# Kernel optimization log

Hardware: AMD Instinct MI355X
Metric: run time of the kernel (lower is better)

## Reference

```python
import jax, jax.numpy as jnp
import numpy as np

EPS = 1e-8


def setup_inputs() -> dict:
    key = jax.random.key(0)
    k1, k2, k3, k4 = jax.random.split(key, 4)
    b, c_in, c_out, h, w_, k = 16, 512, 512, 64, 64, 3
    return {
        "x": jax.random.normal(k1, (b, c_in, h, w_), dtype=jnp.float32),
        "w": jax.random.normal(k2, (b, 512), dtype=jnp.float32),
        "weight": jax.random.normal(k3, (c_out, c_in, k, k), dtype=jnp.float32),
        "affine_w": jax.random.normal(k4, (c_in, 512), dtype=jnp.float32) * 0.02,
        "affine_b": jnp.zeros((c_in,), dtype=jnp.float32),
    }


def reference(x, w, weight, affine_w, affine_b):
    # x: [b, c_in, h, w]; w: [b, 512]; weight: [c_out, c_in, k, k]
    b = x.shape[0]
    # per-sample modulation scale: [b, c_in]
    s = w @ affine_w.T + affine_b + 1.0
    # modulated weights: [b, c_out, c_in, k, k]
    wgt = weight[None] * s[:, None, :, None, None]
    # demodulation: rsqrt of sum over (c_in, kh, kw)
    d = jax.lax.rsqrt(jnp.sum(wgt ** 2, axis=(2, 3, 4)) + EPS)  # [b, c_out]
    wgt = wgt * d[:, :, None, None, None]

    def conv_one(x_i, w_i):
        # x_i: [c_in, h, w] -> [1, c_in, h, w]; w_i: [c_out, c_in, k, k]
        out = jax.lax.conv_general_dilated(
            x_i[None], w_i, window_strides=(1, 1), padding="SAME",
            dimension_numbers=("NCHW", "OIHW", "NCHW"))
        return out[0]

    return jax.vmap(conv_one)(x, wgt)  # [b, c_out, h, w]
```

## Files before the change

kernel.cpp:

```cpp
#include <hip/hip_runtime.h>
#include <cstdint>

typedef __bf16 bf16_t;
typedef __attribute__((ext_vector_type(8))) __bf16 bf16x8;
typedef __attribute__((ext_vector_type(4))) float f32x4;

#define MC_EPS 1e-8f

__device__ __forceinline__ void async_ld16(const bf16_t* g, bf16_t* l) {
  __builtin_amdgcn_global_load_lds(
      (const __attribute__((address_space(1))) void*)g,
      (__attribute__((address_space(3))) void*)l, 16, 0, 0);
}

__global__ void s_kernel(const float* __restrict__ w, const float* __restrict__ aw,
                         const float* __restrict__ ab, float* __restrict__ s) {
  int ci = blockIdx.x, tid = threadIdx.x;
  int b = tid >> 4, part = tid & 15;
  const float* ar = aw + (ci << 9);
  const float* wr = w + (b << 9);
  float acc = 0.f;
  for (int j = part; j < 512; j += 16) acc += wr[j] * ar[j];
  for (int off = 8; off; off >>= 1) acc += __shfl_down(acc, off, 64);
  if (part == 0) s[(b << 9) + ci] = acc + ab[ci] + 1.0f;
}

__global__ void prep_w_kernel(const float* __restrict__ wgt, float* __restrict__ wsq,
                              bf16_t* __restrict__ w_t) {
  int idx = blockIdx.x * 256 + threadIdx.x;
  const float* p = wgt + (size_t)idx * 9;
  float v[9];
  float a = 0.f;
#pragma unroll
  for (int j = 0; j < 9; ++j) { v[j] = p[j]; a += v[j] * v[j]; }
  wsq[idx] = a;
#pragma unroll
  for (int j = 0; j < 9; ++j) w_t[((size_t)j << 18) + idx] = (bf16_t)v[j];
}

__global__ void d_kernel(const float* __restrict__ wsq, const float* __restrict__ s,
                         float* __restrict__ d) {
  int co = blockIdx.x, tid = threadIdx.x;
  int b = tid >> 4, part = tid & 15;
  const float* wr = wsq + (co << 9);
  const float* sr = s + (b << 9);
  float acc = 0.f;
  for (int j = part; j < 512; j += 16) { float sv = sr[j]; acc += wr[j] * sv * sv; }
  for (int off = 8; off; off >>= 1) acc += __shfl_down(acc, off, 64);
  if (part == 0) d[(b << 9) + co] = rsqrtf(acc + MC_EPS);
}

__global__ void halo_kernel(bf16_t* __restrict__ xp) {
  int gid = blockIdx.x * 256 + threadIdx.x;
  if (gid >= 16 * 260 * 64) return;
  int cg = gid & 63;
  int p = (gid >> 6) % 260;
  int b = (gid >> 6) / 260;
  int h, w;
  if (p < 66)       { h = 0;       w = p; }
  else if (p < 132) { h = 65;      w = p - 66; }
  else if (p < 196) { h = p - 131; w = 0; }
  else              { h = p - 195; w = 65; }
  uint4 z = {0u, 0u, 0u, 0u};
  *(uint4*)&xp[((size_t)(b * 66 + h) * 66 + w) * 512 + (cg << 3)] = z;
}

__global__ void xmod_kernel(const float* __restrict__ x, const float* __restrict__ s,
                            bf16_t* __restrict__ xp) {
  int b = blockIdx.x >> 6, h = blockIdx.x & 63;
  int tid = threadIdx.x;
  __shared__ __align__(16) bf16_t tile[64 * 130];
  for (int c0 = 0; c0 < 512; c0 += 128) {
    if (c0) __syncthreads();
    int w4 = (tid & 15) << 2;
    int cl = tid >> 4;
#pragma unroll
    for (int r = 0; r < 8; ++r) {
      int ci = cl + (r << 4);
      const float4 v = *(const float4*)&x[(size_t)(((b << 9) + c0 + ci) << 12) + (h << 6) + w4];
      float sv = s[(b << 9) + c0 + ci];
      tile[(w4 + 0) * 130 + ci] = (bf16_t)(v.x * sv);
      tile[(w4 + 1) * 130 + ci] = (bf16_t)(v.y * sv);
      tile[(w4 + 2) * 130 + ci] = (bf16_t)(v.z * sv);
      tile[(w4 + 3) * 130 + ci] = (bf16_t)(v.w * sv);
    }
    __syncthreads();
#pragma unroll
    for (int it = 0; it < 4; ++it) {
      int i = tid + it * 256;
      int w = i >> 4, cg = i & 15;
      const uint32_t* tp = (const uint32_t*)&tile[w * 130 + (cg << 3)];
      uint4 v = { tp[0], tp[1], tp[2], tp[3] };
      *(uint4*)&xp[((size_t)(b * 66 + h + 1) * 66 + (w + 1)) * 512 + c0 + (cg << 3)] = v;
    }
  }
}

__global__ __launch_bounds__(256) void conv_kernel(
    const bf16_t* __restrict__ xp, const bf16_t* __restrict__ w_t,
    const float* __restrict__ d, float* __restrict__ out) {
  __shared__ __align__(16) bf16_t smem[16384];
  const int tid = threadIdx.x, lane = tid & 63;
  const int g = blockIdx.x;
  const int xcd = g & 7;
  const int slot = g >> 3;
  const int mb = (xcd << 6) + (slot >> 2);
  const int nb = slot & 3;
  const int b = mb >> 5;
  const int h0 = (mb & 31) << 1;
  const int n0 = nb << 7;
  const int wv = tid >> 6, wm = wv >> 1, wn = wv & 1;
  const int quad = lane >> 4, lr = lane & 15;

  f32x4 acc[4][4];
#pragma unroll
  for (int i = 0; i < 4; ++i)
#pragma unroll
    for (int j = 0; j < 4; ++j) acc[i][j] = (f32x4){0.f, 0.f, 0.f, 0.f};

  for (int t = 0; t < 9; ++t) {
    const int kh = t / 3, kw = t % 3;
    for (int ci0 = 0; ci0 < 512; ci0 += 64) {
      __syncthreads();
#pragma unroll
      for (int it = 0; it < 4; ++it) {
        int i = tid + (it << 8);
        int pix = i >> 3;
        int kk = (((i & 7) ^ (pix & 7)) << 3);
        int hp = h0 + (pix >> 6) + kh;
        int wp = (pix & 63) + kw;
        const bf16_t* gp = xp + (((size_t)(b * 66 + hp) * 66 + wp) << 9) + ci0 + kk;
        async_ld16(gp, &smem[(i & ~63) << 3]);
      }
#pragma unroll
      for (int it = 0; it < 4; ++it) {
        int i = tid + (it << 8);
        int n = i >> 3;
        int kk = (((i & 7) ^ (n & 7)) << 3);
        const bf16_t* gp = w_t + (((size_t)((t << 9) + n0 + n)) << 9) + ci0 + kk;
        async_ld16(gp, &smem[8192 + ((i & ~63) << 3)]);
      }
      __syncthreads();
#pragma unroll
      for (int s = 0; s < 2; ++s) {
        bf16x8 af[4], bfr[4];
        const int phys = (((s << 2) | quad) ^ (lr & 7)) << 3;
#pragma unroll
        for (int mt = 0; mt < 4; ++mt)
          af[mt] = *(const bf16x8*)&smem[(((wm << 6) + (mt << 4) + lr) << 6) + phys];
#pragma unroll
        for (int nt = 0; nt < 4; ++nt)
          bfr[nt] = *(const bf16x8*)&smem[8192 + (((wn << 6) + (nt << 4) + lr) << 6) + phys];
#pragma unroll
        for (int mt = 0; mt < 4; ++mt)
#pragma unroll
          for (int nt = 0; nt < 4; ++nt)
            acc[mt][nt] = __builtin_amdgcn_mfma_f32_16x16x32_bf16(af[mt], bfr[nt], acc[mt][nt], 0, 0, 0);
      }
    }
  }

#pragma unroll
  for (int nt = 0; nt < 4; ++nt) {
    const int n = n0 + (wn << 6) + (nt << 4) + lr;
    const float dv = d[(b << 9) + n];
#pragma unroll
    for (int mt = 0; mt < 4; ++mt) {
#pragma unroll
      for (int r = 0; r < 4; ++r) {
        int m = (wm << 6) + (mt << 4) + (quad << 2) + r;
        int h = h0 + (m >> 6), w = m & 63;
        out[((size_t)((b << 9) + n) << 12) + (h << 6) + w] = acc[mt][nt][r] * dv;
      }
    }
  }
}

extern "C" void kernel_launch(void* const* d_in, const int* in_sizes, int n_in,
                              void* d_out, int out_size, void* d_ws, size_t ws_size,
                              hipStream_t stream) {
  const float* x      = (const float*)d_in[0];
  const float* w      = (const float*)d_in[1];
  const float* weight = (const float*)d_in[2];
  const float* aw     = (const float*)d_in[3];
  const float* ab     = (const float*)d_in[4];
  float* out = (float*)d_out;

  char* ws = (char*)d_ws;
  const size_t XP_BYTES  = (size_t)16 * 66 * 66 * 512 * 2;
  const size_t WT_BYTES  = (size_t)9 * 512 * 512 * 2;
  bf16_t* xp   = (bf16_t*)ws;
  bf16_t* w_t  = (bf16_t*)(ws + XP_BYTES);
  float*  s    = (float*)(ws + XP_BYTES + WT_BYTES);
  float*  wsq  = (float*)(ws + XP_BYTES + WT_BYTES + 32768);
  float*  dbuf = (float*)(ws + XP_BYTES + WT_BYTES + 32768 + 1048576);

  halo_kernel<<<1040, 256, 0, stream>>>(xp);
  s_kernel<<<512, 256, 0, stream>>>(w, aw, ab, s);
  prep_w_kernel<<<1024, 256, 0, stream>>>(weight, wsq, w_t);
  d_kernel<<<512, 256, 0, stream>>>(wsq, s, dbuf);
  xmod_kernel<<<1024, 256, 0, stream>>>(x, s, xp);
  conv_kernel<<<2048, 256, 0, stream>>>(xp, w_t, dbuf, out);
}
```

Baseline: 558.6 us.

## Triple-buffer conv LDS tiles with async prefetch and enlarge block tile

Rewrites the implicit-GEMM conv main loop as a flat 72-step K loop over three rotating LDS stages in dynamic shared memory. Global-to-LDS async loads for step k+2 are split across the two MFMA half-steps, with vmcnt waits replacing the full-barrier load/compute serialization. The block grows to 512 threads covering 4 output rows by 128 channels, and setprio is raised around the MFMA bursts. This hides memory latency and amortizes weight loads, but 144 KiB of LDS allows only one block per CU, which lowers occupancy.

```diff
diff --git a/kernel.cpp b/kernel.cpp
--- a/kernel.cpp
+++ b/kernel.cpp
@@ -96,68 +96,119 @@
   }
 }
 
-__global__ __launch_bounds__(256) void conv_kernel(
+__global__ __launch_bounds__(512, 1) void conv_kernel(
     const bf16_t* __restrict__ xp, const bf16_t* __restrict__ w_t,
     const float* __restrict__ d, float* __restrict__ out) {
-  __shared__ __align__(16) bf16_t smem[16384];
+  extern __shared__ bf16_t smem[];
   const int tid = threadIdx.x, lane = tid & 63;
   const int g = blockIdx.x;
   const int xcd = g & 7;
   const int slot = g >> 3;
-  const int mb = (xcd << 6) + (slot >> 2);
+  const int mb = (xcd << 5) + (slot >> 2);
   const int nb = slot & 3;
-  const int b = mb >> 5;
-  const int h0 = (mb & 31) << 1;
+  const int b = mb >> 4;
+  const int h0 = (mb & 15) << 2;
   const int n0 = nb << 7;
   const int wv = tid >> 6, wm = wv >> 1, wn = wv & 1;
   const int quad = lane >> 4, lr = lane & 15;
 
+  size_t a_src[4]; int a_dst[4];
+#pragma unroll
+  for (int j = 0; j < 4; ++j) {
+    int e = (j << 9) + tid;
+    int p = e >> 3;
+    int kk = ((e & 7) ^ (p & 7)) << 3;
+    a_src[j] = ((size_t)((b * 66 + h0 + (p >> 6)) * 66 + (p & 63)) << 9) + kk;
+    a_dst[j] = (e & ~63) << 3;
+  }
+  size_t b_src[2]; int b_dst[2];
+#pragma unroll
+  for (int j = 0; j < 2; ++j) {
+    int e = (j << 9) + tid;
+    int n = e >> 3;
+    int kk = ((e & 7) ^ (n & 7)) << 3;
+    b_src[j] = ((size_t)(n0 + n) << 9) + kk;
+    b_dst[j] = 16384 + ((e & ~63) << 3);
+  }
+
   f32x4 acc[4][4];
 #pragma unroll
   for (int i = 0; i < 4; ++i)
 #pragma unroll
     for (int j = 0; j < 4; ++j) acc[i][j] = (f32x4){0.f, 0.f, 0.f, 0.f};
 
-  for (int t = 0; t < 9; ++t) {
-    const int kh = t / 3, kw = t % 3;
-    for (int ci0 = 0; ci0 < 512; ci0 += 64) {
-      __syncthreads();
-#pragma unroll
-      for (int it = 0; it < 4; ++it) {
-        int i = tid + (it << 8);
-        int pix = i >> 3;
-        int kk = (((i & 7) ^ (pix & 7)) << 3);
-        int hp = h0 + (pix >> 6) + kh;
-        int wp = (pix & 63) + kw;
-        const bf16_t* gp = xp + (((size_t)(b * 66 + hp) * 66 + wp) << 9) + ci0 + kk;
-        async_ld16(gp, &smem[(i & ~63) << 3]);
-      }
-#pragma unroll
-      for (int it = 0; it < 4; ++it) {
-        int i = tid + (it << 8);
-        int n = i >> 3;
-        int kk = (((i & 7) ^ (n & 7)) << 3);
-        const bf16_t* gp = w_t + (((size_t)((t << 9) + n0 + n)) << 9) + ci0 + kk;
-        async_ld16(gp, &smem[8192 + ((i & ~63) << 3)]);
-      }
-      __syncthreads();
-#pragma unroll
-      for (int s = 0; s < 2; ++s) {
-        bf16x8 af[4], bfr[4];
-        const int phys = (((s << 2) | quad) ^ (lr & 7)) << 3;
-#pragma unroll
-        for (int mt = 0; mt < 4; ++mt)
-          af[mt] = *(const bf16x8*)&smem[(((wm << 6) + (mt << 4) + lr) << 6) + phys];
-#pragma unroll
-        for (int nt = 0; nt < 4; ++nt)
-          bfr[nt] = *(const bf16x8*)&smem[8192 + (((wn << 6) + (nt << 4) + lr) << 6) + phys];
-#pragma unroll
-        for (int mt = 0; mt < 4; ++mt)
-#pragma unroll
-          for (int nt = 0; nt < 4; ++nt)
-            acc[mt][nt] = __builtin_amdgcn_mfma_f32_16x16x32_bf16(af[mt], bfr[nt], acc[mt][nt], 0, 0, 0);
-      }
-    }
+#pragma unroll
+  for (int j = 0; j < 4; ++j) async_ld16(xp + a_src[j], &smem[a_dst[j]]);
+#pragma unroll
+  for (int j = 0; j < 2; ++j) async_ld16(w_t + b_src[j], &smem[b_dst[j]]);
+#pragma unroll
+  for (int j = 0; j < 4; ++j) async_ld16(xp + a_src[j] + 64, &smem[24576 + a_dst[j]]);
+#pragma unroll
+  for (int j = 0; j < 2; ++j) async_ld16(w_t + b_src[j] + 64, &smem[24576 + b_dst[j]]);
+  asm volatile("s_waitcnt vmcnt(6)" ::: "memory");
+  __builtin_amdgcn_s_barrier();
+
+  int rs = 0;
+  for (int k = 0; k < 72; ++k) {
+    const int abase = rs * 24576;
+    const int bbase = abase + 16384;
+    const int kp = k + 2;
+    const int rp = (rs == 0) ? 2 : rs - 1;
+    const int pbase = rp * 24576;
+    const int tp = kp >> 3;
+    const int khp = tp / 3, kwp = tp - khp * 3;
+    const size_t a_off = ((size_t)(khp * 66 + kwp) << 9) + ((kp & 7) << 6);
+    const size_t b_off = ((size_t)tp << 18) + ((kp & 7) << 6);
+    const bool pf = kp < 72;
+
+    bf16x8 af[4], bfr[4];
+#pragma unroll
+    for (int mt = 0; mt < 4; ++mt)
+      af[mt] = *(const bf16x8*)&smem[abase + (((wm << 6) + (mt << 4) + lr) << 6) +
+                                     ((quad ^ (lr & 7)) << 3)];
+#pragma unroll
+    for (int nt = 0; nt < 4; ++nt)
+      bfr[nt] = *(const bf16x8*)&smem[bbase + (((wn << 6) + (nt << 4) + lr) << 6) +
+                                      ((quad ^ (lr & 7)) << 3)];
+    if (pf) {
+      async_ld16(xp + a_src[0] + a_off, &smem[pbase + a_dst[0]]);
+      async_ld16(xp + a_src[1] + a_off, &smem[pbase + a_dst[1]]);
+      async_ld16(xp + a_src[2] + a_off, &smem[pbase + a_dst[2]]);
+    }
+    __builtin_amdgcn_s_barrier();
+    __builtin_amdgcn_s_setprio(1);
+#pragma unroll
+    for (int mt = 0; mt < 4; ++mt)
+#pragma unroll
+      for (int nt = 0; nt < 4; ++nt)
+        acc[mt][nt] = __builtin_amdgcn_mfma_f32_16x16x32_bf16(af[mt], bfr[nt], acc[mt][nt], 0, 0, 0);
+    __builtin_amdgcn_s_setprio(0);
+    __builtin_amdgcn_s_barrier();
+#pragma unroll
+    for (int mt = 0; mt < 4; ++mt)
+      af[mt] = *(const bf16x8*)&smem[abase + (((wm << 6) + (mt << 4) + lr) << 6) +
+                                     (((4 | quad) ^ (lr & 7)) << 3)];
+#pragma unroll
+    for (int nt = 0; nt < 4; ++nt)
+      bfr[nt] = *(const bf16x8*)&smem[bbase + (((wn << 6) + (nt << 4) + lr) << 6) +
+                                      (((4 | quad) ^ (lr & 7)) << 3)];
+    if (pf) {
+      async_ld16(xp + a_src[3] + a_off, &smem[pbase + a_dst[3]]);
+      async_ld16(w_t + b_src[0] + b_off, &smem[pbase + b_dst[0]]);
+      async_ld16(w_t + b_src[1] + b_off, &smem[pbase + b_dst[1]]);
+    }
+    __builtin_amdgcn_s_barrier();
+    __builtin_amdgcn_s_setprio(1);
+#pragma unroll
+    for (int mt = 0; mt < 4; ++mt)
+#pragma unroll
+      for (int nt = 0; nt < 4; ++nt)
+        acc[mt][nt] = __builtin_amdgcn_mfma_f32_16x16x32_bf16(af[mt], bfr[nt], acc[mt][nt], 0, 0, 0);
+    __builtin_amdgcn_s_setprio(0);
+    if (k < 70) asm volatile("s_waitcnt vmcnt(6)" ::: "memory");
+    else        asm volatile("s_waitcnt vmcnt(0)" ::: "memory");
+    __builtin_amdgcn_s_barrier();
+    rs = (rs == 2) ? 0 : rs + 1;
   }
 
 #pragma unroll
@@ -195,10 +246,17 @@
   float*  wsq  = (float*)(ws + XP_BYTES + WT_BYTES + 32768);
   float*  dbuf = (float*)(ws + XP_BYTES + WT_BYTES + 32768 + 1048576);
 
+  static int attr_done = 0;
+  if (!attr_done) {
+    hipFuncSetAttribute(reinterpret_cast<const void*>(conv_kernel),
+                        hipFuncAttributeMaxDynamicSharedMemorySize, 147456);
+    attr_done = 1;
+  }
+
   halo_kernel<<<1040, 256, 0, stream>>>(xp);
   s_kernel<<<512, 256, 0, stream>>>(w, aw, ab, s);
   prep_w_kernel<<<1024, 256, 0, stream>>>(weight, wsq, w_t);
   d_kernel<<<512, 256, 0, stream>>>(wsq, s, dbuf);
   xmod_kernel<<<1024, 256, 0, stream>>>(x, s, xp);
-  conv_kernel<<<2048, 256, 0, stream>>>(xp, w_t, dbuf, out);
-}
+  conv_kernel<<<1024, 512, 147456, stream>>>(xp, w_t, dbuf, out);
+}
```

Result: no change. 550.6 us (-1.4%).

## Enlarge conv tile to 256x256 with 4-stage async LDS pipeline

Applied to the files above, without the earlier changes.

The implicit-GEMM conv kernel is restructured from 128x128 tiles with 256 threads and two barriers per 64-wide K step into 256x256 tiles with 512 threads (8 waves, 128x64 per wave). It adds a 4-stage ring of 32-wide K slices in 128KB of dynamic LDS, with global-to-LDS loads issued three stages ahead and a single barrier per step gated by explicit vmcnt waits. The goal is to hide global load latency behind MFMA work and raise arithmetic intensity per byte loaded. The cost is much higher register and LDS use per block, fewer blocks (512) and a tighter dependence on hand-written wait counts being correct.

```diff
diff --git a/kernel.cpp b/kernel.cpp
--- a/kernel.cpp
+++ b/kernel.cpp
@@ -96,68 +96,103 @@
   }
 }
 
-__global__ __launch_bounds__(256) void conv_kernel(
+__global__ __launch_bounds__(512, 2) void conv_kernel(
     const bf16_t* __restrict__ xp, const bf16_t* __restrict__ w_t,
     const float* __restrict__ d, float* __restrict__ out) {
-  __shared__ __align__(16) bf16_t smem[16384];
+  extern __shared__ bf16_t smem[];
   const int tid = threadIdx.x, lane = tid & 63;
   const int g = blockIdx.x;
   const int xcd = g & 7;
   const int slot = g >> 3;
-  const int mb = (xcd << 6) + (slot >> 2);
-  const int nb = slot & 3;
-  const int b = mb >> 5;
-  const int h0 = (mb & 31) << 1;
-  const int n0 = nb << 7;
-  const int wv = tid >> 6, wm = wv >> 1, wn = wv & 1;
+  const int mb = (xcd << 5) + (slot >> 1);
+  const int nb = slot & 1;
+  const int b = mb >> 4;
+  const int h0 = (mb & 15) << 2;
+  const int n0 = nb << 8;
+  const int wv = tid >> 6;
+  const int wm = wv >> 2, wn = wv & 3;
   const int quad = lane >> 4, lr = lane & 15;
 
-  f32x4 acc[4][4];
-#pragma unroll
-  for (int i = 0; i < 4; ++i)
+  int a_base[2], a_dst[2], b_base[2], b_dst[2];
+#pragma unroll
+  for (int j = 0; j < 2; ++j) {
+    int e = (j << 9) + tid;
+    int p = e >> 2;
+    int cig = (e & 3) ^ ((p >> 1) & 3);
+    a_base[j] = ((b * 66 + h0 + (p >> 6)) * 66 + (p & 63)) * 512 + (cig << 3);
+    a_dst[j] = (e & ~63) << 3;
+    b_base[j] = ((n0 + p) << 9) + (cig << 3);
+    b_dst[j] = 8192 + a_dst[j];
+  }
+
+  f32x4 acc[8][4];
+#pragma unroll
+  for (int i = 0; i < 8; ++i)
 #pragma unroll
     for (int j = 0; j < 4; ++j) acc[i][j] = (f32x4){0.f, 0.f, 0.f, 0.f};
 
-  for (int t = 0; t < 9; ++t) {
-    const int kh = t / 3, kw = t % 3;
-    for (int ci0 = 0; ci0 < 512; ci0 += 64) {
-      __syncthreads();
-#pragma unroll
-      for (int it = 0; it < 4; ++it) {
-        int i = tid + (it << 8);
-        int pix = i >> 3;
-        int kk = (((i & 7) ^ (pix & 7)) << 3);
-        int hp = h0 + (pix >> 6) + kh;
-        int wp = (pix & 63) + kw;
-        const bf16_t* gp = xp + (((size_t)(b * 66 + hp) * 66 + wp) << 9) + ci0 + kk;
-        async_ld16(gp, &smem[(i & ~63) << 3]);
-      }
-#pragma unroll
-      for (int it = 0; it < 4; ++it) {
-        int i = tid + (it << 8);
-        int n = i >> 3;
-        int kk = (((i & 7) ^ (n & 7)) << 3);
-        const bf16_t* gp = w_t + (((size_t)((t << 9) + n0 + n)) << 9) + ci0 + kk;
-        async_ld16(gp, &smem[8192 + ((i & ~63) << 3)]);
-      }
-      __syncthreads();
-#pragma unroll
-      for (int s = 0; s < 2; ++s) {
-        bf16x8 af[4], bfr[4];
-        const int phys = (((s << 2) | quad) ^ (lr & 7)) << 3;
-#pragma unroll
-        for (int mt = 0; mt < 4; ++mt)
-          af[mt] = *(const bf16x8*)&smem[(((wm << 6) + (mt << 4) + lr) << 6) + phys];
-#pragma unroll
-        for (int nt = 0; nt < 4; ++nt)
-          bfr[nt] = *(const bf16x8*)&smem[8192 + (((wn << 6) + (nt << 4) + lr) << 6) + phys];
-#pragma unroll
-        for (int mt = 0; mt < 4; ++mt)
-#pragma unroll
-          for (int nt = 0; nt < 4; ++nt)
-            acc[mt][nt] = __builtin_amdgcn_mfma_f32_16x16x32_bf16(af[mt], bfr[nt], acc[mt][nt], 0, 0, 0);
-      }
-    }
+#pragma unroll
+  for (int kt = 0; kt < 3; ++kt) {
+    const int cio = kt << 5;
+    const int sb = kt << 14;
+    async_ld16(xp + a_base[0] + cio, &smem[sb + a_dst[0]]);
+    async_ld16(xp + a_base[1] + cio, &smem[sb + a_dst[1]]);
+    async_ld16(w_t + b_base[0] + cio, &smem[sb + b_dst[0]]);
+    async_ld16(w_t + b_base[1] + cio, &smem[sb + b_dst[1]]);
+  }
+  asm volatile("s_waitcnt vmcnt(8)" ::: "memory");
+  __builtin_amdgcn_s_barrier();
+
+  const int arow = (wm << 7) + lr;
+  const int brow = (wn << 6) + lr;
+  const int phys = (quad ^ ((lr >> 1) & 3)) << 3;
+
+  for (int k = 0; k < 144; ++k) {
+    const int sb = (k & 3) << 14;
+    const int kp = k + 3;
+    const int pb = (kp & 3) << 14;
+    const bool pf = kp < 144;
+    int aoff = 0, boff = 0;
+    if (pf) {
+      const int tp = kp >> 4;
+      const int khp = tp / 3, kwp = tp - khp * 3;
+      aoff = ((khp * 66 + kwp) << 9) + ((kp & 15) << 5);
+      boff = (tp << 18) + ((kp & 15) << 5);
+    }
+
+    bf16x8 af0[4], af1[4], bfr[4];
+#pragma unroll
+    for (int nt = 0; nt < 4; ++nt)
+      bfr[nt] = *(const bf16x8*)&smem[sb + 8192 + ((brow + (nt << 4)) << 5) + phys];
+#pragma unroll
+    for (int mt = 0; mt < 4; ++mt)
+      af0[mt] = *(const bf16x8*)&smem[sb + ((arow + (mt << 4)) << 5) + phys];
+#pragma unroll
+    for (int mt = 0; mt < 4; ++mt)
+      af1[mt] = *(const bf16x8*)&smem[sb + ((arow + 64 + (mt << 4)) << 5) + phys];
+    if (pf) {
+      async_ld16(xp + a_base[0] + aoff, &smem[pb + a_dst[0]]);
+      async_ld16(xp + a_base[1] + aoff, &smem[pb + a_dst[1]]);
+    }
+#pragma unroll
+    for (int mt = 0; mt < 4; ++mt)
+#pragma unroll
+      for (int nt = 0; nt < 4; ++nt)
+        acc[mt][nt] = __builtin_amdgcn_mfma_f32_16x16x32_bf16(af0[mt], bfr[nt], acc[mt][nt], 0, 0, 0);
+    if (pf) {
+      async_ld16(w_t + b_base[0] + boff, &smem[pb + b_dst[0]]);
+      async_ld16(w_t + b_base[1] + boff, &smem[pb + b_dst[1]]);
+    }
+#pragma unroll
+    for (int mt = 0; mt < 4; ++mt)
+#pragma unroll
+      for (int nt = 0; nt < 4; ++nt)
+        acc[4 + mt][nt] = __builtin_amdgcn_mfma_f32_16x16x32_bf16(af1[mt], bfr[nt], acc[4 + mt][nt], 0, 0, 0);
+
+    if (k < 141)      asm volatile("s_waitcnt vmcnt(8)" ::: "memory");
+    else if (k == 141) asm volatile("s_waitcnt vmcnt(4)" ::: "memory");
+    else              asm volatile("s_waitcnt vmcnt(0)" ::: "memory");
+    __builtin_amdgcn_s_barrier();
   }
 
 #pragma unroll
@@ -165,10 +200,10 @@
     const int n = n0 + (wn << 6) + (nt << 4) + lr;
     const float dv = d[(b << 9) + n];
 #pragma unroll
-    for (int mt = 0; mt < 4; ++mt) {
+    for (int mt = 0; mt < 8; ++mt) {
 #pragma unroll
       for (int r = 0; r < 4; ++r) {
-        int m = (wm << 6) + (mt << 4) + (quad << 2) + r;
+        int m = (wm << 7) + (mt << 4) + (quad << 2) + r;
         int h = h0 + (m >> 6), w = m & 63;
         out[((size_t)((b << 9) + n) << 12) + (h << 6) + w] = acc[mt][nt][r] * dv;
       }
@@ -195,10 +230,17 @@
   float*  wsq  = (float*)(ws + XP_BYTES + WT_BYTES + 32768);
   float*  dbuf = (float*)(ws + XP_BYTES + WT_BYTES + 32768 + 1048576);
 
+  static int attr_done = 0;
+  if (!attr_done) {
+    hipFuncSetAttribute(reinterpret_cast<const void*>(conv_kernel),
+                        hipFuncAttributeMaxDynamicSharedMemorySize, 131072);
+    attr_done = 1;
+  }
+
   halo_kernel<<<1040, 256, 0, stream>>>(xp);
   s_kernel<<<512, 256, 0, stream>>>(w, aw, ab, s);
   prep_w_kernel<<<1024, 256, 0, stream>>>(weight, wsq, w_t);
   d_kernel<<<512, 256, 0, stream>>>(wsq, s, dbuf);
   xmod_kernel<<<1024, 256, 0, stream>>>(x, s, xp);
-  conv_kernel<<<2048, 256, 0, stream>>>(xp, w_t, dbuf, out);
-}
+  conv_kernel<<<512, 512, 131072, stream>>>(xp, w_t, dbuf, out);
+}
```

Result: faster. 525.7 us (-5.9%).
